# Kernel tuning notes

Hardware: AMD Instinct MI355X
Metric: run time of the kernel (lower is better)

Reference implementation:

```python
import jax, jax.numpy as jnp
import numpy as np
from jax import lax

SIGMA = 1.0
SIGMA_CUTOFF = 2.0
TAU = 1.0
EPS = 1e-6


def _gauss_kernel1d(sigma=SIGMA, cutoff=SIGMA_CUTOFF):
    r = int(round(cutoff * sigma))
    x = np.arange(-r, r + 1, dtype=np.float32)
    k = np.exp(-(x ** 2) / (2.0 * sigma ** 2))
    return jnp.asarray(k / k.sum())


def _smooth3d(x, k1d):
    # x: [1, 3, D, H, W]; separable depthwise Gaussian along each spatial axis
    k = k1d.shape[0]
    for axis in range(3):
        shape = [1, 1, 1]
        shape[axis] = k
        w = jnp.broadcast_to(k1d.reshape(shape), (3, 1) + tuple(shape))  # [3,1,kd,kh,kw]
        x = lax.conv_general_dilated(
            x, w, window_strides=(1, 1, 1), padding='SAME',
            feature_group_count=3,
            dimension_numbers=('NCDHW', 'OIDHW', 'NCDHW'))
    return x


def setup_inputs() -> dict:
    key = jax.random.key(0)
    k1, k2 = jax.random.split(key)
    shape = (1, 1, 128, 160, 160)
    moving_image = jax.random.normal(k1, shape, dtype=jnp.float32)
    fixed_image = jax.random.normal(k2, shape, dtype=jnp.float32)
    return {"moving_image": moving_image, "fixed_image": fixed_image, "iterations": 10}


def reference(moving_image, fixed_image, iterations):
    mov = moving_image[0, 0]  # [D,H,W]
    fix = fixed_image[0, 0]
    D, H, W = mov.shape
    dtype = mov.dtype
    grid = jnp.stack(jnp.meshgrid(
        jnp.arange(D, dtype=dtype),
        jnp.arange(H, dtype=dtype),
        jnp.arange(W, dtype=dtype), indexing='ij'))  # [3,D,H,W]
    grad_fixed = jnp.stack(jnp.gradient(fix))  # [3,D,H,W] (passive gradient, precomputed)
    k1d = _gauss_kernel1d()

    def warp(vf):
        coords = grid + vf
        return jax.scipy.ndimage.map_coordinates(
            mov, [coords[0], coords[1], coords[2]], order=1, mode='constant', cval=0.0)

    def step(vf, _):
        warped = warp(vf)                      # trilinear spatial transformer
        diff = warped - fix                    # intensity difference
        grad_warped = jnp.stack(jnp.gradient(warped))
        g = grad_warped + grad_fixed           # 'dual' demons gradient
        denom = jnp.sum(g * g, axis=0) + diff * diff
        scale = jnp.where(denom > EPS, -diff / denom, 0.0)  # demon force magnitude
        forces = scale[None] * g               # [3,D,H,W]
        vf = vf + TAU * forces                 # vector-field update
        vf = _smooth3d(vf[None], k1d)[0]       # Gaussian regularization
        return vf, None

    vf0 = jnp.zeros((3, D, H, W), dtype=dtype)
    vf, _ = lax.scan(step, vf0, None, length=iterations)
    return vf[None]  # [1,3,D,H,W]
```

## Files before the change

### kernel.cpp

```cpp
#include <hip/hip_runtime.h>
#include <math.h>

#define D_ 128
#define H_ 160
#define W_ 160
#define NVOX (D_*H_*W_)
#define HW (H_*W_)
#define N4 (NVOX/4)

#define K0 0.40261996f
#define K1 0.24420134f
#define K2 0.05448868f

union F4 { float4 v; float a[4]; };

__device__ __forceinline__ float4 zero4() { float4 z; z.x=z.y=z.z=z.w=0.f; return z; }
__device__ __forceinline__ float4 bcast4(float x) { float4 r; r.x=r.y=r.z=r.w=x; return r; }

__device__ __forceinline__ float fetch_mov(const float* __restrict__ m, int d, int h, int w) {
    if ((unsigned)d >= (unsigned)D_ || (unsigned)h >= (unsigned)H_ || (unsigned)w >= (unsigned)W_) return 0.0f;
    return m[(size_t)(d*H_ + h)*W_ + w];
}

__device__ __forceinline__ float trilerp(const float* __restrict__ mov,
                                         float cd, float ch, float cw) {
    float fd = floorf(cd), fh = floorf(ch), fw = floorf(cw);
    int di = (int)fd, hi = (int)fh, wi = (int)fw;
    float td = cd - fd, th = ch - fh, tw = cw - fw;
    float c000, c001, c010, c011, c100, c101, c110, c111;
    if (di >= 0 && di < D_-1 && hi >= 0 && hi < H_-1 && wi >= 0 && wi < W_-1) {
        const float* p = mov + (size_t)di*HW + hi*W_ + wi;
        c000 = p[0];    c001 = p[1];
        c010 = p[W_];   c011 = p[W_+1];
        const float* q = p + HW;
        c100 = q[0];    c101 = q[1];
        c110 = q[W_];   c111 = q[W_+1];
    } else {
        c000 = fetch_mov(mov, di,   hi,   wi  );
        c001 = fetch_mov(mov, di,   hi,   wi+1);
        c010 = fetch_mov(mov, di,   hi+1, wi  );
        c011 = fetch_mov(mov, di,   hi+1, wi+1);
        c100 = fetch_mov(mov, di+1, hi,   wi  );
        c101 = fetch_mov(mov, di+1, hi,   wi+1);
        c110 = fetch_mov(mov, di+1, hi+1, wi  );
        c111 = fetch_mov(mov, di+1, hi+1, wi+1);
    }
    float c00 = c000 + tw*(c001 - c000);
    float c01 = c010 + tw*(c011 - c010);
    float c10 = c100 + tw*(c101 - c100);
    float c11 = c110 + tw*(c111 - c110);
    float c0 = c00 + th*(c01 - c00);
    float c1 = c10 + th*(c11 - c10);
    return c0 + td*(c1 - c0);
}

#define UROW 48

__global__ __launch_bounds__(256, 4) void force_wh_kernel(const float* __restrict__ warped,
                                                          const float* __restrict__ fix,
                                                          const float* __restrict__ vf,
                                                          float* __restrict__ tout,
                                                          int zero_vf) {
    __shared__ float u[3][36][UROW];
    __shared__ float tw[38][48];
    __shared__ float tf[38][48];
    const int tx = threadIdx.x;
    const int ty = threadIdx.y;
    const int tid = ty*8 + tx;
    const int bswz = (blockIdx.x & 7)*400 + (blockIdx.x >> 3);
    const int d   = bswz / 25;
    const int rem = bswz % 25;
    const int h0 = (rem / 5) * 32;
    const int w0 = (rem % 5) * 32;

    #define UF4(ch, r, fc) (((float4*)&u[(ch)][(r)][0]) + ((fc) ^ ((r)&3)))

    for (int s = tid; s < 456; s += 256) {
        int R  = s / 12, C4 = s % 12;
        int gh = h0 - 3 + R;
        int ghc = gh < 0 ? 0 : (gh > H_-1 ? H_-1 : gh);
        int gw = w0 - 8 + 4*C4;
        size_t rb = (size_t)d*HW + (size_t)ghc*W_;
        float4 wv, fv;
        if (gw < 0) {
            wv = bcast4(warped[rb]);  fv = bcast4(fix[rb]);
        } else if (gw + 4 > W_) {
            wv = bcast4(warped[rb + W_-1]); fv = bcast4(fix[rb + W_-1]);
        } else {
            wv = *(const float4*)(warped + rb + gw);
            fv = *(const float4*)(fix    + rb + gw);
        }
        *(float4*)&tw[R][4*C4] = wv;
        *(float4*)&tf[R][4*C4] = fv;
    }
    __syncthreads();

    for (int slot = tid; slot < 360; slot += 256) {
        int r = slot/10, c = slot%10;
        int gh = h0 - 2 + r;
        int gw = w0 - 4 + 4*c;
        F4 o0, o1, o2;
        if ((unsigned)gh < (unsigned)H_ && gw >= 0 && gw + 4 <= W_) {
            size_t base = (size_t)d*HW + (size_t)gh*W_ + gw;
            int i4 = (int)(base >> 2);
            int up = (d < D_-1) ?  (HW/4) : 0;
            int dn = (d > 0)    ? -(HW/4) : 0;
            const float4* w4p = (const float4*)warped;
            const float4* f4p = (const float4*)fix;
            F4 du, dnv, fdu, fdn;
            du.v  = w4p[i4 + up];
            dnv.v = w4p[i4 + dn];
            fdu.v = f4p[i4 + up];
            fdn.v = f4p[i4 + dn];
            if (zero_vf) {
                o0.v = zero4(); o1.v = zero4(); o2.v = zero4();
            } else {
                o0.v = ((const float4*)vf)[i4];
                o1.v = ((const float4*)vf)[i4 + N4];
                o2.v = ((const float4*)vf)[i4 + 2*N4];
            }
            int sr = r + 1, sc = 4*c + 4;
            F4 cc, fc, hu, hd, fhu, fhd;
            cc.v  = *(const float4*)&tw[sr  ][sc];
            fc.v  = *(const float4*)&tf[sr  ][sc];
            hu.v  = *(const float4*)&tw[sr+1][sc];
            hd.v  = *(const float4*)&tw[sr-1][sc];
            fhu.v = *(const float4*)&tf[sr+1][sc];
            fhd.v = *(const float4*)&tf[sr-1][sc];
            float cl = tw[sr][sc-1], cr = tw[sr][sc+4];
            float fl = tf[sr][sc-1], fr = tf[sr][sc+4];
            float hs  = (gh==0 || gh==H_-1) ? 1.f : 0.5f;
            float dsc = (d==0  || d==D_-1)  ? 1.f : 0.5f;
            float m [6] = {cl, cc.a[0], cc.a[1], cc.a[2], cc.a[3], cr};
            float fm[6] = {fl, fc.a[0], fc.a[1], fc.a[2], fc.a[3], fr};
            #pragma unroll
            for (int j = 0; j < 4; ++j) {
                int wj = gw + j;
                float wsc  = (wj == 0 || wj == W_-1) ? 1.f : 0.5f;
                float prev  = (wj == 0)    ? m[1]  : m[j];
                float next  = (wj == W_-1) ? m[4]  : m[j+2];
                float fprev = (wj == 0)    ? fm[1] : fm[j];
                float fnext = (wj == W_-1) ? fm[4] : fm[j+2];
                float G0 = dsc*(du.a[j] - dnv.a[j]) + dsc*(fdu.a[j] - fdn.a[j]);
                float G1 = hs *(hu.a[j] - hd.a[j])  + hs *(fhu.a[j] - fhd.a[j]);
                float G2 = wsc*(next - prev)        + wsc*(fnext - fprev);
                float diff = cc.a[j] - fc.a[j];
                float denom = G0*G0 + G1*G1 + G2*G2 + diff*diff;
                float scale = (denom > 1e-6f) ? (-diff/denom) : 0.0f;
                o0.a[j] += scale*G0;
                o1.a[j] += scale*G1;
                o2.a[j] += scale*G2;
            }
        } else {
            o0.v = zero4(); o1.v = zero4(); o2.v = zero4();
        }
        *UF4(0, r, c) = o0.v;
        *UF4(1, r, c) = o1.v;
        *UF4(2, r, c) = o2.v;
    }
    __syncthreads();

    F4 wout[4];
    int jch = 0, jr = 0, jh = 0;
    const bool has = (tid < 216);
    if (has) {
        jch = tid / 72;
        int rem2 = tid % 72;
        jr = rem2 >> 1;
        jh = rem2 & 1;
        F4 q[6];
        #pragma unroll
        for (int i = 0; i < 6; ++i) q[i].v = *UF4(jch, jr, 4*jh + i);
        float mm[24];
        #pragma unroll
        for (int i = 0; i < 6; ++i) {
            mm[4*i+0]=q[i].a[0]; mm[4*i+1]=q[i].a[1]; mm[4*i+2]=q[i].a[2]; mm[4*i+3]=q[i].a[3];
        }
        #pragma unroll
        for (int o = 0; o < 16; ++o)
            wout[o>>2].a[o&3] = K2*(mm[o+2]+mm[o+6]) + K1*(mm[o+3]+mm[o+5]) + K0*mm[o+4];
    }
    __syncthreads();

    if (has) {
        #pragma unroll
        for (int f = 0; f < 4; ++f) *UF4(jch, jr, 4*jh + f) = wout[f].v;
    }
    __syncthreads();

    size_t base = (size_t)d*HW + (h0+ty)*W_ + w0 + 4*tx;
    #pragma unroll
    for (int ch = 0; ch < 3; ++ch) {
        F4 q0, q1, q2, q3, q4;
        q0.v = *UF4(ch, ty  , tx);
        q1.v = *UF4(ch, ty+1, tx);
        q2.v = *UF4(ch, ty+2, tx);
        q3.v = *UF4(ch, ty+3, tx);
        q4.v = *UF4(ch, ty+4, tx);
        float4 s2;
        s2.x = K2*(q0.a[0]+q4.a[0]) + K1*(q1.a[0]+q3.a[0]) + K0*q2.a[0];
        s2.y = K2*(q0.a[1]+q4.a[1]) + K1*(q1.a[1]+q3.a[1]) + K0*q2.a[1];
        s2.z = K2*(q0.a[2]+q4.a[2]) + K1*(q1.a[2]+q3.a[2]) + K0*q2.a[2];
        s2.w = K2*(q0.a[3]+q4.a[3]) + K1*(q1.a[3]+q3.a[3]) + K0*q2.a[3];
        *(float4*)(tout + (size_t)ch*NVOX + base) = s2;
    }
    #undef UF4
}

__global__ __launch_bounds__(256) void smooth_d_warp_kernel(const float* __restrict__ t,
                                                            const float* __restrict__ mov,
                                                            float* __restrict__ vf_out,
                                                            float* __restrict__ warped_out,
                                                            int do_warp) {
    const int chunk = (blockIdx.x & 7)*400 + (blockIdx.x >> 3);
    int i4 = chunk*256 + (int)threadIdx.x;
    if (i4 >= N4) return;
    int base = 4*i4;
    int w = base % W_;
    int h = (base / W_) % H_;
    int d = base / HW;
    F4 va[3];
    #pragma unroll
    for (int ch = 0; ch < 3; ++ch) {
        const float4* tp = (const float4*)(t + (size_t)ch*NVOX);
        float4 q0 = (d >= 2)    ? tp[i4 - HW/2] : zero4();
        float4 q1 = (d >= 1)    ? tp[i4 - HW/4] : zero4();
        float4 q2 = tp[i4];
        float4 q3 = (d < D_-1)  ? tp[i4 + HW/4] : zero4();
        float4 q4 = (d < D_-2)  ? tp[i4 + HW/2] : zero4();
        va[ch].a[0] = K2*(q0.x+q4.x) + K1*(q1.x+q3.x) + K0*q2.x;
        va[ch].a[1] = K2*(q0.y+q4.y) + K1*(q1.y+q3.y) + K0*q2.y;
        va[ch].a[2] = K2*(q0.z+q4.z) + K1*(q1.z+q3.z) + K0*q2.z;
        va[ch].a[3] = K2*(q0.w+q4.w) + K1*(q1.w+q3.w) + K0*q2.w;
    }
    ((float4*)vf_out)[i4]        = va[0].v;
    ((float4*)vf_out)[i4 + N4]   = va[1].v;
    ((float4*)vf_out)[i4 + 2*N4] = va[2].v;
    if (do_warp) {
        F4 r4o;
        #pragma unroll
        for (int j = 0; j < 4; ++j) {
            float cd = (float)d       + va[0].a[j];
            float ch = (float)h       + va[1].a[j];
            float cw = (float)(w + j) + va[2].a[j];
            r4o.a[j] = trilerp(mov, cd, ch, cw);
        }
        ((float4*)warped_out)[i4] = r4o.v;
    }
}

extern "C" void kernel_launch(void* const* d_in, const int* in_sizes, int n_in,
                              void* d_out, int out_size, void* d_ws, size_t ws_size,
                              hipStream_t stream) {
    const float* mov = (const float*)d_in[0];
    const float* fix = (const float*)d_in[1];
    const int ITERS = 10;

    float* ws     = (float*)d_ws;
    float* vfA    = ws;
    float* tbuf   = ws + (size_t)3*NVOX;
    float* warped = ws + (size_t)6*NVOX;

    const int nblk = 3200;

    for (int it = 0; it < ITERS; ++it) {
        const float* wsrc = (it == 0) ? mov : warped;
        force_wh_kernel<<<dim3(nblk), dim3(8,32), 0, stream>>>(wsrc, fix, vfA, tbuf,
                                                               it == 0 ? 1 : 0);
        float* vdst = (it == ITERS-1) ? (float*)d_out : vfA;
        smooth_d_warp_kernel<<<dim3(nblk), dim3(256), 0, stream>>>(tbuf, mov, vdst, warped,
                                                                   it == ITERS-1 ? 0 : 1);
    }
}
```

Baseline: 582.2 us.

## Compute four depth slices per thread in D-smoothing kernel with register sliding window

Each thread in the depth-smoothing-and-warp kernel now produces four consecutive depth slices for one float4 column. It keeps a sliding window of input planes in registers, loading 8 planes per channel instead of 20, and the grid shrinks from 3200 to 800 blocks. This cuts redundant global loads of the temporary buffer. In exchange it raises register pressure and lowers the number of threads available to hide trilinear gather latency.

New measurement: 645.4 us. 1.11x slower.

```diff
diff --git a/kernel.cpp b/kernel.cpp
--- a/kernel.cpp
+++ b/kernel.cpp
@@ -7,6 +7,7 @@
 #define NVOX (D_*H_*W_)
 #define HW (H_*W_)
 #define N4 (NVOX/4)
+#define HW4 (HW/4)
 
 #define K0 0.40261996f
 #define K1 0.24420134f
@@ -212,40 +213,87 @@
                                                             float* __restrict__ vf_out,
                                                             float* __restrict__ warped_out,
                                                             int do_warp) {
-    const int chunk = (blockIdx.x & 7)*400 + (blockIdx.x >> 3);
-    int i4 = chunk*256 + (int)threadIdx.x;
-    if (i4 >= N4) return;
-    int base = 4*i4;
-    int w = base % W_;
-    int h = (base / W_) % H_;
-    int d = base / HW;
-    F4 va[3];
+    const int chunk = (blockIdx.x & 7)*100 + (blockIdx.x >> 3);
+    const int col = chunk*256 + (int)threadIdx.x;
+    const int hw4 = col % HW4;
+    const int d0  = (col / HW4) * 4;
+    const int w = (hw4 % (W_/4)) * 4;
+    const int h = hw4 / (W_/4);
+
+    F4 q[3][6];
     #pragma unroll
     for (int ch = 0; ch < 3; ++ch) {
         const float4* tp = (const float4*)(t + (size_t)ch*NVOX);
-        float4 q0 = (d >= 2)    ? tp[i4 - HW/2] : zero4();
-        float4 q1 = (d >= 1)    ? tp[i4 - HW/4] : zero4();
-        float4 q2 = tp[i4];
-        float4 q3 = (d < D_-1)  ? tp[i4 + HW/4] : zero4();
-        float4 q4 = (d < D_-2)  ? tp[i4 + HW/2] : zero4();
-        va[ch].a[0] = K2*(q0.x+q4.x) + K1*(q1.x+q3.x) + K0*q2.x;
-        va[ch].a[1] = K2*(q0.y+q4.y) + K1*(q1.y+q3.y) + K0*q2.y;
-        va[ch].a[2] = K2*(q0.z+q4.z) + K1*(q1.z+q3.z) + K0*q2.z;
-        va[ch].a[3] = K2*(q0.w+q4.w) + K1*(q1.w+q3.w) + K0*q2.w;
-    }
-    ((float4*)vf_out)[i4]        = va[0].v;
-    ((float4*)vf_out)[i4 + N4]   = va[1].v;
-    ((float4*)vf_out)[i4 + 2*N4] = va[2].v;
-    if (do_warp) {
-        F4 r4o;
-        #pragma unroll
-        for (int j = 0; j < 4; ++j) {
-            float cd = (float)d       + va[0].a[j];
-            float ch = (float)h       + va[1].a[j];
-            float cw = (float)(w + j) + va[2].a[j];
-            r4o.a[j] = trilerp(mov, cd, ch, cw);
-        }
-        ((float4*)warped_out)[i4] = r4o.v;
+        #pragma unroll
+        for (int i = 0; i < 6; ++i) {
+            int p = d0 - 2 + i;
+            q[ch][i].v = ((unsigned)p < (unsigned)D_) ? tp[p*HW4 + hw4] : zero4();
+        }
+    }
+    #pragma unroll
+    for (int k = 0; k < 2; ++k) {
+        F4 va[3];
+        #pragma unroll
+        for (int ch = 0; ch < 3; ++ch) {
+            #pragma unroll
+            for (int j = 0; j < 4; ++j)
+                va[ch].a[j] = K2*(q[ch][k].a[j]+q[ch][k+4].a[j])
+                            + K1*(q[ch][k+1].a[j]+q[ch][k+3].a[j])
+                            + K0*q[ch][k+2].a[j];
+        }
+        int i4 = (d0+k)*HW4 + hw4;
+        ((float4*)vf_out)[i4]        = va[0].v;
+        ((float4*)vf_out)[i4 + N4]   = va[1].v;
+        ((float4*)vf_out)[i4 + 2*N4] = va[2].v;
+        if (do_warp) {
+            F4 r4o;
+            #pragma unroll
+            for (int j = 0; j < 4; ++j) {
+                float cd = (float)(d0+k) + va[0].a[j];
+                float ch2 = (float)h      + va[1].a[j];
+                float cw = (float)(w + j) + va[2].a[j];
+                r4o.a[j] = trilerp(mov, cd, ch2, cw);
+            }
+            ((float4*)warped_out)[i4] = r4o.v;
+        }
+    }
+    #pragma unroll
+    for (int ch = 0; ch < 3; ++ch) {
+        const float4* tp = (const float4*)(t + (size_t)ch*NVOX);
+        #pragma unroll
+        for (int i = 0; i < 4; ++i) q[ch][i] = q[ch][i+2];
+        #pragma unroll
+        for (int i = 4; i < 6; ++i) {
+            int p = d0 + i;
+            q[ch][i].v = ((unsigned)p < (unsigned)D_) ? tp[p*HW4 + hw4] : zero4();
+        }
+    }
+    #pragma unroll
+    for (int k = 2; k < 4; ++k) {
+        F4 va[3];
+        #pragma unroll
+        for (int ch = 0; ch < 3; ++ch) {
+            #pragma unroll
+            for (int j = 0; j < 4; ++j)
+                va[ch].a[j] = K2*(q[ch][k-2].a[j]+q[ch][k+2].a[j])
+                            + K1*(q[ch][k-1].a[j]+q[ch][k+1].a[j])
+                            + K0*q[ch][k].a[j];
+        }
+        int i4 = (d0+k)*HW4 + hw4;
+        ((float4*)vf_out)[i4]        = va[0].v;
+        ((float4*)vf_out)[i4 + N4]   = va[1].v;
+        ((float4*)vf_out)[i4 + 2*N4] = va[2].v;
+        if (do_warp) {
+            F4 r4o;
+            #pragma unroll
+            for (int j = 0; j < 4; ++j) {
+                float cd = (float)(d0+k) + va[0].a[j];
+                float ch2 = (float)h      + va[1].a[j];
+                float cw = (float)(w + j) + va[2].a[j];
+                r4o.a[j] = trilerp(mov, cd, ch2, cw);
+            }
+            ((float4*)warped_out)[i4] = r4o.v;
+        }
     }
 }
 
@@ -261,14 +309,12 @@
     float* tbuf   = ws + (size_t)3*NVOX;
     float* warped = ws + (size_t)6*NVOX;
 
-    const int nblk = 3200;
-
     for (int it = 0; it < ITERS; ++it) {
         const float* wsrc = (it == 0) ? mov : warped;
-        force_wh_kernel<<<dim3(nblk), dim3(8,32), 0, stream>>>(wsrc, fix, vfA, tbuf,
+        force_wh_kernel<<<dim3(3200), dim3(8,32), 0, stream>>>(wsrc, fix, vfA, tbuf,
                                                                it == 0 ? 1 : 0);
         float* vdst = (it == ITERS-1) ? (float*)d_out : vfA;
-        smooth_d_warp_kernel<<<dim3(nblk), dim3(256), 0, stream>>>(tbuf, mov, vdst, warped,
-                                                                   it == ITERS-1 ? 0 : 1);
-    }
-}
+        smooth_d_warp_kernel<<<dim3(800), dim3(256), 0, stream>>>(tbuf, mov, vdst, warped,
+                                                                  it == ITERS-1 ? 0 : 1);
+    }
+}
```
